# Kernel optimization log

Measured on AMD Instinct MI355X. Metric: run time of the kernel, lower is better.

Reference implementation:

```python
import jax, jax.numpy as jnp
import numpy as np

B, L, C, R = 4, 2048, 64, 8
A_SCALE = 0.1  # keeps spectral radius of per-step A < 1 so 2048-step products stay stable


def setup_inputs() -> dict:
    key = jax.random.key(0)
    k1, k2, k3, k4 = jax.random.split(key, 4)
    A_re = jax.random.normal(k1, (B, L, C, R, R), jnp.float32) * A_SCALE
    A_im = jax.random.normal(k2, (B, L, C, R, R), jnp.float32) * A_SCALE
    X_re = jax.random.normal(k3, (B, L, C, R), jnp.float32)
    X_im = jax.random.normal(k4, (B, L, C, R), jnp.float32)
    return {"A_re": A_re, "A_im": A_im, "X_re": X_re, "X_im": X_im}


def reference(A_re, A_im, X_re, X_im):
    # Complex linear recurrence: Y_t = A_t @ Y_{t-1} + X_t (Y_0 = X_0),
    # computed as a parallel associative scan over the L axis, matching
    # the Triton combine_fn: (a1,x1) o (a2,x2) = (a2@a1, a2@x1 + x2).
    A = jax.lax.complex(A_re, A_im)  # [B,L,C,R,R] complex64
    X = jax.lax.complex(X_re, X_im)  # [B,L,C,R]   complex64

    def combine(left, right):
        a1, x1 = left
        a2, x2 = right
        new_a = jnp.matmul(a2, a1)                          # [.,R,R]@[.,R,R]
        new_x = jnp.einsum('...ij,...j->...i', a2, x1) + x2  # [.,R,R]@[.,R]
        return (new_a, new_x)

    _, Y = jax.lax.associative_scan(combine, (A, X), axis=1)
    # Return real/imag stacked so the output dtype is float32: [B,L,C,R,2]
    return jnp.stack((jnp.real(Y), jnp.imag(Y)), axis=-1)
```

## Files before the change

kernel.cpp:

```cpp
#include <hip/hip_runtime.h>

#define B 4
#define L 2048
#define C 64
#define R 8
#define NCH (B * C)
#define TQ 64
#define S (L / TQ)
#define GRP (NCH / 8)


__global__ __launch_bounds__(64) void k_summary(
    const float* __restrict__ Are, const float* __restrict__ Aim,
    const float* __restrict__ Xre, const float* __restrict__ Xim,
    float2* __restrict__ sumP, float2* __restrict__ sumQ)
{
    __shared__ __align__(16) float sm[1152];
    const int lane = threadIdx.x;
    const int c = lane >> 3, r = lane & 7;
    const int s = blockIdx.x >> 5;
    const int g = blockIdx.x & 31;
    const int n0 = g * 8;
    const int b = n0 >> 6;
    const int cc0 = n0 & (C - 1);
    const int n = n0 + c;
    const int tbase = s * TQ;

    float Pre[8], Pim[8];
#pragma unroll
    for (int k = 0; k < 8; ++k) { Pre[k] = (k == r) ? 1.f : 0.f; Pim[k] = 0.f; }
    float qre = 0.f, qim = 0.f;

    float4 sa0, sa1, si0, si1; float sxr, sxi;
    float4 ta0, ta1, ti0, ti1; float txr, txi;

#define LOADSET1(t, A0, A1, I0, I1, XR, XI)                                    \
    {                                                                          \
        const int fb = (b * L + (t)) * C + cc0;                                \
        const float4* pA = (const float4*)(Are + (long)fb * 64) + lane * 2;    \
        const float4* pI = (const float4*)(Aim + (long)fb * 64) + lane * 2;    \
        A0 = pA[0]; A1 = pA[1]; I0 = pI[0]; I1 = pI[1];                        \
        XR = Xre[(long)fb * 8 + lane]; XI = Xim[(long)fb * 8 + lane];          \
    }

#define STAGESET1(A0, A1, I0, I1, XR, XI)                                      \
    {                                                                          \
        float4* s4 = (float4*)sm;                                              \
        s4[lane * 2] = A0; s4[lane * 2 + 1] = A1;                              \
        s4[128 + lane * 2] = I0; s4[128 + lane * 2 + 1] = I1;                  \
        sm[1024 + lane] = XR; sm[1088 + lane] = XI;                            \
    }

#define COMPUTE_STEP1()                                                        \
    {                                                                          \
        float xr[8], xi[8];                                                    \
        *(float4*)&xr[0] = *(const float4*)(sm + 1024 + c * 8);                \
        *(float4*)&xr[4] = *(const float4*)(sm + 1024 + c * 8 + 4);            \
        *(float4*)&xi[0] = *(const float4*)(sm + 1088 + c * 8);                \
        *(float4*)&xi[4] = *(const float4*)(sm + 1088 + c * 8 + 4);            \
        _Pragma("unroll")                                                      \
        for (int k = 0; k < 8; ++k) {                                          \
            qre += Pre[k] * xr[k] - Pim[k] * xi[k];                            \
            qim += Pre[k] * xi[k] + Pim[k] * xr[k];                            \
        }                                                                      \
        float Nre[8], Nim[8];                                                  \
        _Pragma("unroll")                                                      \
        for (int j = 0; j < 8; ++j) { Nre[j] = 0.f; Nim[j] = 0.f; }            \
        _Pragma("unroll")                                                      \
        for (int k = 0; k < 8; ++k) {                                          \
            float er[8], ei[8];                                                \
            *(float4*)&er[0] = *(const float4*)(sm + c * 64 + k * 8);          \
            *(float4*)&er[4] = *(const float4*)(sm + c * 64 + k * 8 + 4);      \
            *(float4*)&ei[0] = *(const float4*)(sm + 512 + c * 64 + k * 8);    \
            *(float4*)&ei[4] = *(const float4*)(sm + 512 + c * 64 + k * 8 + 4);\
            const float pr = Pre[k], pi = Pim[k];                              \
            _Pragma("unroll")                                                  \
            for (int j = 0; j < 8; ++j) {                                      \
                Nre[j] += pr * er[j] - pi * ei[j];                             \
                Nim[j] += pr * ei[j] + pi * er[j];                             \
            }                                                                  \
        }                                                                      \
        _Pragma("unroll")                                                      \
        for (int k = 0; k < 8; ++k) { Pre[k] = Nre[k]; Pim[k] = Nim[k]; }      \
    }

    LOADSET1(tbase + TQ - 1, sa0, sa1, si0, si1, sxr, sxi);
    LOADSET1(tbase + TQ - 2, ta0, ta1, ti0, ti1, txr, txi);

#pragma unroll 1
    for (int tt = TQ - 1; tt >= 1; tt -= 2) {
        STAGESET1(sa0, sa1, si0, si1, sxr, sxi);
        if (tt >= 3) LOADSET1(tbase + tt - 2, sa0, sa1, si0, si1, sxr, sxi);
        COMPUTE_STEP1();
        STAGESET1(ta0, ta1, ti0, ti1, txr, txi);
        if (tt >= 3) LOADSET1(tbase + tt - 3, ta0, ta1, ti0, ti1, txr, txi);
        COMPUTE_STEP1();
    }

    float4* gp = (float4*)(sumP + ((long)(s * 256 + n) * 8 + r) * 8);
    gp[0] = make_float4(Pre[0], Pim[0], Pre[1], Pim[1]);
    gp[1] = make_float4(Pre[2], Pim[2], Pre[3], Pim[3]);
    gp[2] = make_float4(Pre[4], Pim[4], Pre[5], Pim[5]);
    gp[3] = make_float4(Pre[6], Pim[6], Pre[7], Pim[7]);
    sumQ[(long)(s * 256 + n) * 8 + r] = make_float2(qre, qim);
}

__global__ __launch_bounds__(64) void k_carry(
    const float2* __restrict__ sumP, const float2* __restrict__ sumQ,
    float2* __restrict__ carry)
{
    __shared__ __align__(16) float cb[128];
    const int lane = threadIdx.x;
    const int c = lane >> 3, r = lane & 7;
    const int n = blockIdx.x * 8 + c;

    float yr = 0.f, yi = 0.f;
#pragma unroll 1
    for (int s = 0; s < S; ++s) {
        const long base = (long)(s * 256 + n) * 8;
        carry[base + r] = make_float2(yr, yi);
        cb[lane * 2] = yr; cb[lane * 2 + 1] = yi;
        float yvr[8], yvi[8];
        {
            float4 u0 = *(const float4*)(cb + c * 16);
            float4 u1 = *(const float4*)(cb + c * 16 + 4);
            float4 u2 = *(const float4*)(cb + c * 16 + 8);
            float4 u3 = *(const float4*)(cb + c * 16 + 12);
            yvr[0]=u0.x; yvi[0]=u0.y; yvr[1]=u0.z; yvi[1]=u0.w;
            yvr[2]=u1.x; yvi[2]=u1.y; yvr[3]=u1.z; yvi[3]=u1.w;
            yvr[4]=u2.x; yvi[4]=u2.y; yvr[5]=u2.z; yvi[5]=u2.w;
            yvr[6]=u3.x; yvi[6]=u3.y; yvr[7]=u3.z; yvi[7]=u3.w;
        }
        const float4* prow = (const float4*)(sumP + (base + r) * 8);
        float4 p0 = prow[0], p1 = prow[1], p2 = prow[2], p3 = prow[3];
        float prr[8], pri[8];
        prr[0]=p0.x; pri[0]=p0.y; prr[1]=p0.z; pri[1]=p0.w;
        prr[2]=p1.x; pri[2]=p1.y; prr[3]=p1.z; pri[3]=p1.w;
        prr[4]=p2.x; pri[4]=p2.y; prr[5]=p2.z; pri[5]=p2.w;
        prr[6]=p3.x; pri[6]=p3.y; prr[7]=p3.z; pri[7]=p3.w;
        float2 qv = sumQ[base + r];
        float nr = qv.x, ni = qv.y;
#pragma unroll
        for (int k = 0; k < 8; ++k) {
            nr += prr[k] * yvr[k] - pri[k] * yvi[k];
            ni += prr[k] * yvi[k] + pri[k] * yvr[k];
        }
        yr = nr; yi = ni;
    }
}

__global__ __launch_bounds__(64) void k_fixup(
    const float* __restrict__ Are, const float* __restrict__ Aim,
    const float* __restrict__ Xre, const float* __restrict__ Xim,
    const float2* __restrict__ carry, float2* __restrict__ out)
{
    __shared__ __align__(16) float sm[1024];
    __shared__ __align__(16) float cb[128];
    const int lane = threadIdx.x;
    const int c = lane >> 3, r = lane & 7;
    const int blk = (int)gridDim.x - 1 - (int)blockIdx.x;
    const int s = blk >> 5;
    const int g = blk & 31;
    const int n0 = g * 8;
    const int b = n0 >> 6;
    const int cc0 = n0 & (C - 1);
    const int n = n0 + c;
    const int tbase = s * TQ;

    float yvr[8], yvi[8];
    {
        const float4* cv = (const float4*)(carry + (long)(s * 256 + n) * 8);
        float4 w0 = cv[0], w1 = cv[1], w2 = cv[2], w3 = cv[3];
        yvr[0]=w0.x; yvi[0]=w0.y; yvr[1]=w0.z; yvi[1]=w0.w;
        yvr[2]=w1.x; yvi[2]=w1.y; yvr[3]=w1.z; yvi[3]=w1.w;
        yvr[4]=w2.x; yvi[4]=w2.y; yvr[5]=w2.z; yvi[5]=w2.w;
        yvr[6]=w3.x; yvi[6]=w3.y; yvr[7]=w3.z; yvi[7]=w3.w;
    }

    float4 sa0, sa1, si0, si1; float sxr, sxi;
    float4 ta0, ta1, ti0, ti1; float txr, txi;

#define LOADSET3(t, A0, A1, I0, I1, XR, XI)                                    \
    {                                                                          \
        const int fb = (b * L + (t)) * C + cc0;                                \
        const float4* pA = (const float4*)(Are + (long)fb * 64) + lane * 2;    \
        const float4* pI = (const float4*)(Aim + (long)fb * 64) + lane * 2;    \
        A0 = pA[0]; A1 = pA[1]; I0 = pI[0]; I1 = pI[1];                        \
        XR = Xre[(long)fb * 8 + lane]; XI = Xim[(long)fb * 8 + lane];          \
    }

#define STAGESET3(A0, A1, I0, I1)                                              \
    {                                                                          \
        float4* s4 = (float4*)sm;                                              \
        s4[lane * 2] = A0; s4[lane * 2 + 1] = A1;                              \
        s4[128 + lane * 2] = I0; s4[128 + lane * 2 + 1] = I1;                  \
    }

#define FIX_STEP(t, XR_, XI_)                                                  \
    {                                                                          \
        float ar[8], ai[8];                                                    \
        *(float4*)&ar[0] = *(const float4*)(sm + c * 64 + r * 8);              \
        *(float4*)&ar[4] = *(const float4*)(sm + c * 64 + r * 8 + 4);          \
        *(float4*)&ai[0] = *(const float4*)(sm + 512 + c * 64 + r * 8);        \
        *(float4*)&ai[4] = *(const float4*)(sm + 512 + c * 64 + r * 8 + 4);    \
        float nr = XR_, ni = XI_;                                              \
        _Pragma("unroll")                                                      \
        for (int k = 0; k < 8; ++k) {                                          \
            nr += ar[k] * yvr[k] - ai[k] * yvi[k];                             \
            ni += ar[k] * yvi[k] + ai[k] * yvr[k];                             \
        }                                                                      \
        const int fb = (b * L + (t)) * C + cc0;                                \
        out[(long)fb * 8 + lane] = make_float2(nr, ni);                        \
        cb[lane * 2] = nr; cb[lane * 2 + 1] = ni;                              \
        float4 u0 = *(const float4*)(cb + c * 16);                             \
        float4 u1 = *(const float4*)(cb + c * 16 + 4);                         \
        float4 u2 = *(const float4*)(cb + c * 16 + 8);                         \
        float4 u3 = *(const float4*)(cb + c * 16 + 12);                        \
        yvr[0]=u0.x; yvi[0]=u0.y; yvr[1]=u0.z; yvi[1]=u0.w;                    \
        yvr[2]=u1.x; yvi[2]=u1.y; yvr[3]=u1.z; yvi[3]=u1.w;                    \
        yvr[4]=u2.x; yvi[4]=u2.y; yvr[5]=u2.z; yvi[5]=u2.w;                    \
        yvr[6]=u3.x; yvi[6]=u3.y; yvr[7]=u3.z; yvi[7]=u3.w;                    \
    }

    LOADSET3(tbase + 0, sa0, sa1, si0, si1, sxr, sxi);
    LOADSET3(tbase + 1, ta0, ta1, ti0, ti1, txr, txi);

#pragma unroll 1
    for (int tt = 0; tt < TQ; tt += 2) {
        STAGESET3(sa0, sa1, si0, si1);
        float xcr = sxr, xci = sxi;
        if (tt + 2 < TQ) LOADSET3(tbase + tt + 2, sa0, sa1, si0, si1, sxr, sxi);
        FIX_STEP(tbase + tt, xcr, xci);
        STAGESET3(ta0, ta1, ti0, ti1);
        float xdr = txr, xdi = txi;
        if (tt + 3 < TQ) LOADSET3(tbase + tt + 3, ta0, ta1, ti0, ti1, txr, txi);
        FIX_STEP(tbase + tt + 1, xdr, xdi);
    }
}

extern "C" void kernel_launch(void* const* d_in, const int* in_sizes, int n_in,
                              void* d_out, int out_size, void* d_ws, size_t ws_size,
                              hipStream_t stream)
{
    const float* Are = (const float*)d_in[0];
    const float* Aim = (const float*)d_in[1];
    const float* Xre = (const float*)d_in[2];
    const float* Xim = (const float*)d_in[3];
    float2* out = (float2*)d_out;

    float2* sumP  = (float2*)d_ws;
    float2* sumQ  = sumP + (long)S * NCH * 64;
    float2* carry = sumQ + (long)S * NCH * 8;

    k_summary<<<S * GRP, 64, 0, stream>>>(Are, Aim, Xre, Xim, sumP, sumQ);
    k_carry<<<NCH / 8, 64, 0, stream>>>(sumP, sumQ, carry);
    k_fixup<<<S * GRP, 64, 0, stream>>>(Are, Aim, Xre, Xim, carry, out);
}
```

Baseline: 379.6 us.

## Shrink scan chunk, swizzle LDS, prefetch carry inputs, drop fixup LDS staging

Cuts the chunk length from 64 to 16 so the summary and fixup kernels launch four times as many blocks and each serial chain is shorter. The longer carry chain is countered by prefetching the next chunk's summary and splitting accumulators into two chains. Also XOR-swizzles the summary LDS layout and pads the carry buffer to avoid bank conflicts. The fixup kernel now uses its loaded A row from registers instead of staging it through LDS, and occupancy hints are added. The trade-off is a carry pass with 128 sequential steps and four times the summary workspace traffic.

```diff
diff --git a/kernel.cpp b/kernel.cpp
--- a/kernel.cpp
+++ b/kernel.cpp
@@ -5,12 +5,12 @@
 #define C 64
 #define R 8
 #define NCH (B * C)
-#define TQ 64
+#define TQ 16
 #define S (L / TQ)
 #define GRP (NCH / 8)
 
 
-__global__ __launch_bounds__(64) void k_summary(
+__global__ __launch_bounds__(64, 4) void k_summary(
     const float* __restrict__ Are, const float* __restrict__ Aim,
     const float* __restrict__ Xre, const float* __restrict__ Xim,
     float2* __restrict__ sumP, float2* __restrict__ sumQ)
@@ -25,6 +25,7 @@
     const int cc0 = n0 & (C - 1);
     const int n = n0 + c;
     const int tbase = s * TQ;
+    const int sIdx = c * 16 + ((r ^ c) << 1);
 
     float Pre[8], Pim[8];
 #pragma unroll
@@ -46,8 +47,8 @@
 #define STAGESET1(A0, A1, I0, I1, XR, XI)                                      \
     {                                                                          \
         float4* s4 = (float4*)sm;                                              \
-        s4[lane * 2] = A0; s4[lane * 2 + 1] = A1;                              \
-        s4[128 + lane * 2] = I0; s4[128 + lane * 2 + 1] = I1;                  \
+        s4[sIdx] = A0; s4[sIdx + 1] = A1;                                      \
+        s4[128 + sIdx] = I0; s4[128 + sIdx + 1] = I1;                          \
         sm[1024 + lane] = XR; sm[1088 + lane] = XI;                            \
     }
 
@@ -68,11 +69,12 @@
         for (int j = 0; j < 8; ++j) { Nre[j] = 0.f; Nim[j] = 0.f; }            \
         _Pragma("unroll")                                                      \
         for (int k = 0; k < 8; ++k) {                                          \
+            const int ko = ((k ^ c) << 3);    \
             float er[8], ei[8];                                                \
-            *(float4*)&er[0] = *(const float4*)(sm + c * 64 + k * 8);          \
-            *(float4*)&er[4] = *(const float4*)(sm + c * 64 + k * 8 + 4);      \
-            *(float4*)&ei[0] = *(const float4*)(sm + 512 + c * 64 + k * 8);    \
-            *(float4*)&ei[4] = *(const float4*)(sm + 512 + c * 64 + k * 8 + 4);\
+            *(float4*)&er[0] = *(const float4*)(sm + c * 64 + ko);             \
+            *(float4*)&er[4] = *(const float4*)(sm + c * 64 + ko + 4);         \
+            *(float4*)&ei[0] = *(const float4*)(sm + 512 + c * 64 + ko);       \
+            *(float4*)&ei[4] = *(const float4*)(sm + 512 + c * 64 + ko + 4);   \
             const float pr = Pre[k], pi = Pim[k];                              \
             _Pragma("unroll")                                                  \
             for (int j = 0; j < 8; ++j) {                                      \
@@ -109,53 +111,64 @@
     const float2* __restrict__ sumP, const float2* __restrict__ sumQ,
     float2* __restrict__ carry)
 {
-    __shared__ __align__(16) float cb[128];
+    __shared__ __align__(16) float cb[160];
     const int lane = threadIdx.x;
     const int c = lane >> 3, r = lane & 7;
     const int n = blockIdx.x * 8 + c;
 
     float yr = 0.f, yi = 0.f;
+    long base = (long)n * 8;
+    const float4* prow0 = (const float4*)(sumP + (base + r) * 8);
+    float4 p0 = prow0[0], p1 = prow0[1], p2 = prow0[2], p3 = prow0[3];
+    float2 qv = sumQ[base + r];
+
 #pragma unroll 1
     for (int s = 0; s < S; ++s) {
-        const long base = (long)(s * 256 + n) * 8;
         carry[base + r] = make_float2(yr, yi);
-        cb[lane * 2] = yr; cb[lane * 2 + 1] = yi;
+        *(float2*)(cb + c * 20 + 2 * r) = make_float2(yr, yi);
+        float4 w0 = p0, w1 = p1, w2 = p2, w3 = p3;
+        float2 q = qv;
+        if (s + 1 < S) {
+            const long nb = base + 2048;
+            const float4* np = (const float4*)(sumP + (nb + r) * 8);
+            p0 = np[0]; p1 = np[1]; p2 = np[2]; p3 = np[3];
+            qv = sumQ[nb + r];
+        }
         float yvr[8], yvi[8];
         {
-            float4 u0 = *(const float4*)(cb + c * 16);
-            float4 u1 = *(const float4*)(cb + c * 16 + 4);
-            float4 u2 = *(const float4*)(cb + c * 16 + 8);
-            float4 u3 = *(const float4*)(cb + c * 16 + 12);
+            float4 u0 = *(const float4*)(cb + c * 20);
+            float4 u1 = *(const float4*)(cb + c * 20 + 4);
+            float4 u2 = *(const float4*)(cb + c * 20 + 8);
+            float4 u3 = *(const float4*)(cb + c * 20 + 12);
             yvr[0]=u0.x; yvi[0]=u0.y; yvr[1]=u0.z; yvi[1]=u0.w;
             yvr[2]=u1.x; yvi[2]=u1.y; yvr[3]=u1.z; yvi[3]=u1.w;
             yvr[4]=u2.x; yvi[4]=u2.y; yvr[5]=u2.z; yvi[5]=u2.w;
             yvr[6]=u3.x; yvi[6]=u3.y; yvr[7]=u3.z; yvi[7]=u3.w;
         }
-        const float4* prow = (const float4*)(sumP + (base + r) * 8);
-        float4 p0 = prow[0], p1 = prow[1], p2 = prow[2], p3 = prow[3];
         float prr[8], pri[8];
-        prr[0]=p0.x; pri[0]=p0.y; prr[1]=p0.z; pri[1]=p0.w;
-        prr[2]=p1.x; pri[2]=p1.y; prr[3]=p1.z; pri[3]=p1.w;
-        prr[4]=p2.x; pri[4]=p2.y; prr[5]=p2.z; pri[5]=p2.w;
-        prr[6]=p3.x; pri[6]=p3.y; prr[7]=p3.z; pri[7]=p3.w;
-        float2 qv = sumQ[base + r];
-        float nr = qv.x, ni = qv.y;
+        prr[0]=w0.x; pri[0]=w0.y; prr[1]=w0.z; pri[1]=w0.w;
+        prr[2]=w1.x; pri[2]=w1.y; prr[3]=w1.z; pri[3]=w1.w;
+        prr[4]=w2.x; pri[4]=w2.y; prr[5]=w2.z; pri[5]=w2.w;
+        prr[6]=w3.x; pri[6]=w3.y; prr[7]=w3.z; pri[7]=w3.w;
+        float nr0 = q.x, ni0 = q.y, nr1 = 0.f, ni1 = 0.f;
 #pragma unroll
-        for (int k = 0; k < 8; ++k) {
-            nr += prr[k] * yvr[k] - pri[k] * yvi[k];
-            ni += prr[k] * yvi[k] + pri[k] * yvr[k];
+        for (int k = 0; k < 8; k += 2) {
+            nr0 += prr[k] * yvr[k] - pri[k] * yvi[k];
+            ni0 += prr[k] * yvi[k] + pri[k] * yvr[k];
+            nr1 += prr[k+1] * yvr[k+1] - pri[k+1] * yvi[k+1];
+            ni1 += prr[k+1] * yvi[k+1] + pri[k+1] * yvr[k+1];
         }
-        yr = nr; yi = ni;
-    }
-}
-
-__global__ __launch_bounds__(64) void k_fixup(
+        yr = nr0 + nr1; yi = ni0 + ni1;
+        base += 2048;
+    }
+}
+
+__global__ __launch_bounds__(64, 4) void k_fixup(
     const float* __restrict__ Are, const float* __restrict__ Aim,
     const float* __restrict__ Xre, const float* __restrict__ Xim,
     const float2* __restrict__ carry, float2* __restrict__ out)
 {
-    __shared__ __align__(16) float sm[1024];
-    __shared__ __align__(16) float cb[128];
+    __shared__ __align__(16) float cb[160];
     const int lane = threadIdx.x;
     const int c = lane >> 3, r = lane & 7;
     const int blk = (int)gridDim.x - 1 - (int)blockIdx.x;
@@ -189,33 +202,33 @@
         XR = Xre[(long)fb * 8 + lane]; XI = Xim[(long)fb * 8 + lane];          \
     }
 
-#define STAGESET3(A0, A1, I0, I1)                                              \
-    {                                                                          \
-        float4* s4 = (float4*)sm;                                              \
-        s4[lane * 2] = A0; s4[lane * 2 + 1] = A1;                              \
-        s4[128 + lane * 2] = I0; s4[128 + lane * 2 + 1] = I1;                  \
-    }
-
-#define FIX_STEP(t, XR_, XI_)                                                  \
-    {                                                                          \
-        float ar[8], ai[8];                                                    \
-        *(float4*)&ar[0] = *(const float4*)(sm + c * 64 + r * 8);              \
-        *(float4*)&ar[4] = *(const float4*)(sm + c * 64 + r * 8 + 4);          \
-        *(float4*)&ai[0] = *(const float4*)(sm + 512 + c * 64 + r * 8);        \
-        *(float4*)&ai[4] = *(const float4*)(sm + 512 + c * 64 + r * 8 + 4);    \
-        float nr = XR_, ni = XI_;                                              \
-        _Pragma("unroll")                                                      \
-        for (int k = 0; k < 8; ++k) {                                          \
-            nr += ar[k] * yvr[k] - ai[k] * yvi[k];                             \
-            ni += ar[k] * yvi[k] + ai[k] * yvr[k];                             \
-        }                                                                      \
+#define FIX_STEP(A0, A1, I0, I1, XR_, XI_, t)                                  \
+    {                                                                          \
+        float nr0 = (XR_), ni0 = (XI_), nr1 = 0.f, ni1 = 0.f;                  \
+        nr0 += A0.x * yvr[0] - I0.x * yvi[0];                                  \
+        ni0 += A0.x * yvi[0] + I0.x * yvr[0];                                  \
+        nr1 += A0.y * yvr[1] - I0.y * yvi[1];                                  \
+        ni1 += A0.y * yvi[1] + I0.y * yvr[1];                                  \
+        nr0 += A0.z * yvr[2] - I0.z * yvi[2];                                  \
+        ni0 += A0.z * yvi[2] + I0.z * yvr[2];                                  \
+        nr1 += A0.w * yvr[3] - I0.w * yvi[3];                                  \
+        ni1 += A0.w * yvi[3] + I0.w * yvr[3];                                  \
+        nr0 += A1.x * yvr[4] - I1.x * yvi[4];                                  \
+        ni0 += A1.x * yvi[4] + I1.x * yvr[4];                                  \
+        nr1 += A1.y * yvr[5] - I1.y * yvi[5];                                  \
+        ni1 += A1.y * yvi[5] + I1.y * yvr[5];                                  \
+        nr0 += A1.z * yvr[6] - I1.z * yvi[6];                                  \
+        ni0 += A1.z * yvi[6] + I1.z * yvr[6];                                  \
+        nr1 += A1.w * yvr[7] - I1.w * yvi[7];                                  \
+        ni1 += A1.w * yvi[7] + I1.w * yvr[7];                                  \
+        const float nr = nr0 + nr1, ni = ni0 + ni1;                            \
         const int fb = (b * L + (t)) * C + cc0;                                \
         out[(long)fb * 8 + lane] = make_float2(nr, ni);                        \
-        cb[lane * 2] = nr; cb[lane * 2 + 1] = ni;                              \
-        float4 u0 = *(const float4*)(cb + c * 16);                             \
-        float4 u1 = *(const float4*)(cb + c * 16 + 4);                         \
-        float4 u2 = *(const float4*)(cb + c * 16 + 8);                         \
-        float4 u3 = *(const float4*)(cb + c * 16 + 12);                        \
+        *(float2*)(cb + c * 20 + 2 * r) = make_float2(nr, ni);                 \
+        float4 u0 = *(const float4*)(cb + c * 20);                             \
+        float4 u1 = *(const float4*)(cb + c * 20 + 4);                         \
+        float4 u2 = *(const float4*)(cb + c * 20 + 8);                         \
+        float4 u3 = *(const float4*)(cb + c * 20 + 12);                        \
         yvr[0]=u0.x; yvi[0]=u0.y; yvr[1]=u0.z; yvi[1]=u0.w;                    \
         yvr[2]=u1.x; yvi[2]=u1.y; yvr[3]=u1.z; yvi[3]=u1.w;                    \
         yvr[4]=u2.x; yvi[4]=u2.y; yvr[5]=u2.z; yvi[5]=u2.w;                    \
@@ -227,14 +240,14 @@
 
 #pragma unroll 1
     for (int tt = 0; tt < TQ; tt += 2) {
-        STAGESET3(sa0, sa1, si0, si1);
-        float xcr = sxr, xci = sxi;
+        float4 A0 = sa0, A1 = sa1, I0 = si0, I1 = si1;
+        float XR = sxr, XI = sxi;
         if (tt + 2 < TQ) LOADSET3(tbase + tt + 2, sa0, sa1, si0, si1, sxr, sxi);
-        FIX_STEP(tbase + tt, xcr, xci);
-        STAGESET3(ta0, ta1, ti0, ti1);
-        float xdr = txr, xdi = txi;
+        FIX_STEP(A0, A1, I0, I1, XR, XI, tbase + tt);
+        float4 B0 = ta0, B1 = ta1, J0 = ti0, J1 = ti1;
+        float YR = txr, YI = txi;
         if (tt + 3 < TQ) LOADSET3(tbase + tt + 3, ta0, ta1, ti0, ti1, txr, txi);
-        FIX_STEP(tbase + tt + 1, xdr, xdi);
+        FIX_STEP(B0, B1, J0, J1, YR, YI, tbase + tt + 1);
     }
 }
 
```

Result: slower. 971.3 us (+155.9%).
